# Kernel optimization log

Hardware: AMD Instinct MI355X
Metric: run time of the kernel (lower is better)

Reference implementation:

```python
import jax, jax.numpy as jnp
import numpy as np

B, L, H, NH = 2, 2048, 2048, 16
K = H // NH  # q/k head dim (num_slot) = 128
EPS = 1e-5
SCALE = K ** -0.5  # fla gla default scale = key_dim**-0.5


def setup_inputs() -> dict:
    key = jax.random.key(0)
    k0, k1, k2, k3, k4 = jax.random.split(key, 5)
    std = 0.02
    return {
        "hidden_states": jax.random.normal(k0, (B, L, H), dtype=jnp.float32),
        "Wq": jax.random.normal(k1, (K, H), dtype=jnp.float32) * std,
        "Wk": jax.random.normal(k2, (K, H), dtype=jnp.float32) * std,
        "Wog": jax.random.normal(k3, (H, H), dtype=jnp.float32) * std,
        "Wig": jax.random.normal(k4, (H, H), dtype=jnp.float32) * std,
        "g_weight": jnp.ones((H,), dtype=jnp.float32),
    }


def _gla(q, k, v, g):
    # q,k: [B,L,K]; v: [B,L,V]; g: [B,L,K] (log decay per key dim)
    # recurrence: S_t = exp(g_t)[:, :, None] * S_{t-1} + k_t^T v_t ; o_t = q_t @ S_t
    def step(S, xs):
        q_t, k_t, v_t, g_t = xs  # [B,K],[B,K],[B,V],[B,K]
        S = jnp.exp(g_t)[:, :, None] * S + k_t[:, :, None] * v_t[:, None, :]
        o_t = jnp.einsum('bk,bkv->bv', q_t, S)
        return S, o_t

    S0 = jnp.zeros((q.shape[0], q.shape[2], v.shape[2]), dtype=q.dtype)
    xs = (jnp.swapaxes(q, 0, 1), jnp.swapaxes(k, 0, 1),
          jnp.swapaxes(v, 0, 1), jnp.swapaxes(g, 0, 1))
    _, o = jax.lax.scan(step, S0, xs)  # o: [L,B,V]
    return jnp.swapaxes(o, 0, 1)


def reference(hidden_states, Wq, Wk, Wog, Wig, g_weight):
    x = hidden_states
    q = x @ Wq.T  # [B,L,K]
    k_sig = jax.nn.sigmoid(x @ Wk.T)  # k = sigmoid(k_proj(x))
    q = jax.nn.silu(q) * SCALE  # swish feature map on q; fold in GLA scale
    gf = jax.nn.log_sigmoid(-k_sig)  # per-key log decay gates
    o = _gla(q, k_sig, x, gf)  # [B,L,H] (single head, V = hidden)
    # output gate + fused RMSNorm-SwishGate
    go = o @ Wog.T + x @ Wig.T
    rms = o * jax.lax.rsqrt(jnp.mean(o * o, axis=-1, keepdims=True) + EPS) * g_weight
    return rms * go * jax.nn.sigmoid(go)
```

## Files before the change

kernel.cpp:

```cpp
#include <hip/hip_runtime.h>
#include <math.h>

#define B_ 2
#define L_ 2048
#define H_ 2048
#define KD_ 128
#define SCALE_ 0.08838834764831845f
#define EPS_ 1e-5f
#define K2_ 4096

typedef __bf16 bf16x8 __attribute__((ext_vector_type(8)));
typedef float f32x4 __attribute__((ext_vector_type(4)));

static __device__ __forceinline__ float sigmoidf_(float z) {
    return 1.0f / (1.0f + __expf(-z));
}

static __device__ __forceinline__ unsigned short f2bf(float f) {
    unsigned int u = __float_as_uint(f);
    unsigned int r = (u + 0x7fffu + ((u >> 16) & 1u)) >> 16;
    return (unsigned short)r;
}

static __device__ __forceinline__ float bf2f(unsigned short s) {
    return __uint_as_float(((unsigned int)s) << 16);
}

#define ASYNC_COPY16(gsrc, ldst)                                             \
    __builtin_amdgcn_global_load_lds(                                        \
        (const __attribute__((address_space(1))) unsigned int*)(gsrc),       \
        (__attribute__((address_space(3))) unsigned int*)(ldst), 16, 0, 0)

#define BAR()                                                                \
    do {                                                                     \
        asm volatile("" ::: "memory");                                       \
        __builtin_amdgcn_s_barrier();                                        \
        asm volatile("" ::: "memory");                                       \
    } while (0)

#define JOBA_BLKS 4096
#define JOBB_BLKS 256
#define JOBC_BLKS 4096

__global__ __launch_bounds__(256) void prep_all(
    const float* __restrict__ x, const float* __restrict__ Wq,
    const float* __restrict__ Wk, const float* __restrict__ Wog,
    const float* __restrict__ Wig, unsigned short* __restrict__ Abuf,
    unsigned short* __restrict__ Wqk, unsigned short* __restrict__ Bbuf,
    float* __restrict__ rrms_acc)
{
    const int blk = blockIdx.x;
    const float* src;
    unsigned short* dst;
    if (blk < JOBA_BLKS) {
        size_t i = (size_t)blk * 256 + threadIdx.x;
        size_t m = i >> 8, c8 = (i & 255) * 8;
        src = x + m * H_ + c8;
        dst = Abuf + m * K2_ + H_ + c8;
    } else if (blk < JOBA_BLKS + JOBB_BLKS) {
        size_t i = (size_t)(blk - JOBA_BLKS) * 256 + threadIdx.x;
        if (i < 4096) rrms_acc[i] = 0.f;
        const size_t half = (size_t)KD_ * H_ / 8;
        src = ((i < half) ? Wq : Wk) + ((i < half) ? i : i - half) * 8;
        dst = Wqk + i * 8;
    } else {
        size_t i = (size_t)(blk - JOBA_BLKS - JOBB_BLKS) * 256 + threadIdx.x;
        const size_t half = (size_t)H_ * H_ / 8;
        size_t j = (i < half) ? i : i - half;
        size_t n = j >> 8, c8 = (j & 255) * 8;
        src = ((i < half) ? Wog : Wig) + n * H_ + c8;
        dst = Bbuf + n * K2_ + ((i < half) ? 0 : H_) + c8;
    }
    float4 v0 = *(const float4*)src;
    float4 v1 = *(const float4*)(src + 4);
    ushort4 a, b;
    a.x = f2bf(v0.x); a.y = f2bf(v0.y); a.z = f2bf(v0.z); a.w = f2bf(v0.w);
    b.x = f2bf(v1.x); b.y = f2bf(v1.y); b.z = f2bf(v1.z); b.w = f2bf(v1.w);
    *(ushort4*)dst = a;
    *(ushort4*)(dst + 4) = b;
}

__global__ __launch_bounds__(512, 2) void qk_proj_mfma(
    const unsigned short* __restrict__ Abuf,
    const unsigned short* __restrict__ Wqk,
    float* __restrict__ partial)
{
    __shared__ alignas(16) unsigned short As[3 * 64 * 64];
    __shared__ alignas(16) unsigned short Bs[3 * 256 * 64];
    const int tid  = threadIdx.x;
    const int lane = tid & 63;
    const int w    = tid >> 6;
    const int wrow = w >> 2;
    const int wcol = w & 3;
    const int bid  = blockIdx.x;
    const int m0 = (bid >> 2) * 64;
    const int kz = (bid & 3) * 512;

    const int frow = lane & 15;
    const int fkb  = (lane >> 4) << 3;
    const int rxor = (lane & 7) << 3;

    const int srow = tid >> 3;
    const int scol = (((tid & 7) ^ (srow & 7)) << 3);
    const unsigned short* agsrc =
        Abuf + (size_t)(m0 + srow) * K2_ + H_ + kz + scol;
    const unsigned short* bgsrc = Wqk + (size_t)srow * H_ + kz + scol;
    unsigned short* As_dst = As + tid * 8;
    unsigned short* Bs_dst = Bs + tid * 8;

#define QSTAGE_A_(cb, k0)                                                    \
    ASYNC_COPY16(agsrc + (k0), As_dst + (cb) * 4096)
#define QSTAGE_B_(cb, k0, it_)                                               \
    ASYNC_COPY16(bgsrc + (size_t)((it_) * 64) * H_ + (k0),                   \
                 Bs_dst + (cb) * 16384 + (it_) * 4096)
#define QLDA_(buf, i_, ks_)                                                  \
    (*(const bf16x8*)(As + (buf) * 4096 +                                    \
                      (wrow * 32 + (i_) * 16 + frow) * 64 +                  \
                      (((ks_) * 32 + fkb) ^ rxor)))
#define QLDB_(buf, j_, ks_)                                                  \
    (*(const bf16x8*)(Bs + (buf) * 16384 +                                   \
                      (wcol * 64 + (j_) * 16 + frow) * 64 +                  \
                      (((ks_) * 32 + fkb) ^ rxor)))
#define MFMA_(a_, b_, c_)                                                    \
    (c_) = __builtin_amdgcn_mfma_f32_16x16x32_bf16((a_), (b_), (c_), 0, 0, 0)

    f32x4 acc[2][4] = {};

    QSTAGE_A_(0, 0);
    QSTAGE_B_(0, 0, 0); QSTAGE_B_(0, 0, 1); QSTAGE_B_(0, 0, 2); QSTAGE_B_(0, 0, 3);
    QSTAGE_A_(1, 64);
    QSTAGE_B_(1, 64, 0); QSTAGE_B_(1, 64, 1); QSTAGE_B_(1, 64, 2); QSTAGE_B_(1, 64, 3);
    asm volatile("s_waitcnt vmcnt(5)" ::: "memory");
    BAR();

    int cur = 0;
    for (int t = 0; t < 8; ++t) {
        int stg = cur + 2; if (stg >= 3) stg -= 3;
        const int kpre = (t + 2) * 64;
        const bool pre = (t + 2 < 8);
        bf16x8 af0[2], bf0[4], af1[2], bf1[4];

        #pragma unroll
        for (int i = 0; i < 2; ++i) af0[i] = QLDA_(cur, i, 0);
        #pragma unroll
        for (int j = 0; j < 4; ++j) bf0[j] = QLDB_(cur, j, 0);
        #pragma unroll
        for (int i = 0; i < 2; ++i) af1[i] = QLDA_(cur, i, 1);
        #pragma unroll
        for (int j = 0; j < 4; ++j) bf1[j] = QLDB_(cur, j, 1);

        if (pre) {
            QSTAGE_A_(stg, kpre);
            QSTAGE_B_(stg, kpre, 0);
            QSTAGE_B_(stg, kpre, 1);
            QSTAGE_B_(stg, kpre, 2);
            QSTAGE_B_(stg, kpre, 3);
        }

        __builtin_amdgcn_s_setprio(1);
        #pragma unroll
        for (int i = 0; i < 2; ++i)
            #pragma unroll
            for (int j = 0; j < 4; ++j)
                MFMA_(af0[i], bf0[j], acc[i][j]);
        #pragma unroll
        for (int i = 0; i < 2; ++i)
            #pragma unroll
            for (int j = 0; j < 4; ++j)
                MFMA_(af1[i], bf1[j], acc[i][j]);
        __builtin_amdgcn_s_setprio(0);

        if (pre) { asm volatile("s_waitcnt vmcnt(5)" ::: "memory"); }
        else     { asm volatile("s_waitcnt vmcnt(0)" ::: "memory"); }
        BAR();

        cur = cur + 1; if (cur == 3) cur = 0;
    }

#undef QSTAGE_A_
#undef QSTAGE_B_
#undef QLDA_
#undef QLDB_
#undef MFMA_

    float* pz = partial + (size_t)(bid & 3) * 4096 * 256;
    #pragma unroll
    for (int i = 0; i < 2; ++i) {
        #pragma unroll
        for (int reg = 0; reg < 4; ++reg) {
            int m = m0 + wrow * 32 + i * 16 + (lane >> 4) * 4 + reg;
            #pragma unroll
            for (int j = 0; j < 4; ++j) {
                int n = wcol * 64 + j * 16 + (lane & 15);
                pz[(size_t)m * 256 + n] = acc[i][j][reg];
            }
        }
    }
}

__global__ __launch_bounds__(256) void scan_scale_kernel(
    const float* __restrict__ partial,
    unsigned short* __restrict__ qt_b, unsigned short* __restrict__ kA_b,
    unsigned short* __restrict__ kB_b)
{
    const int c = blockIdx.x, b = blockIdx.y;
    const int kd = blockIdx.z * 32 + (threadIdx.x & 31);
    const int rg = threadIdx.x >> 5;
    const size_t stride = (size_t)4096 * 256;
    const int row0 = b * L_ + c * 64 + rg * 8;

    float qv[8], kv[8], gp[8];
    float run = 0.f;
    #pragma unroll
    for (int j = 0; j < 8; ++j) {
        size_t off = (size_t)(row0 + j) * 256;
        float sq = partial[off + kd] + partial[stride + off + kd]
                 + partial[2 * stride + off + kd] + partial[3 * stride + off + kd];
        float sk = partial[off + 128 + kd] + partial[stride + off + 128 + kd]
                 + partial[2 * stride + off + 128 + kd]
                 + partial[3 * stride + off + 128 + kd];
        float ksv = sigmoidf_(sk);
        qv[j] = sq * sigmoidf_(sq) * SCALE_;
        kv[j] = ksv;
        run += -log1pf(__expf(ksv));
        gp[j] = run;
    }
    __shared__ float s_seg[8][32];
    s_seg[rg][threadIdx.x & 31] = run;
    __syncthreads();
    float base = 0.f, total = 0.f;
    #pragma unroll
    for (int r = 0; r < 8; ++r) {
        float v = s_seg[r][threadIdx.x & 31];
        base += (r < rg) ? v : 0.f;
        total += v;
    }
    #pragma unroll
    for (int j = 0; j < 8; ++j) {
        float s = base + gp[j];
        size_t idx = (size_t)(row0 + j) * KD_ + kd;
        qt_b[idx] = f2bf(qv[j] * __expf(s));
        kA_b[idx] = f2bf(kv[j] * __expf(-s));
        kB_b[idx] = f2bf(kv[j] * __expf(total - s));
    }
}

#define SV_ 130
#define SP_ 136

__global__ __launch_bounds__(256) void pv_fused(
    const unsigned short* __restrict__ qt_b,
    const unsigned short* __restrict__ kA_b,
    const unsigned short* __restrict__ kB_b,
    unsigned short* Abuf,
    float* __restrict__ rrms_acc)
{
    const int c  = blockIdx.x;
    const int b  = blockIdx.y;
    const int vg = blockIdx.z;
    const int tid = threadIdx.x;
    const int w = tid >> 6, l = tid & 63;
    const int lr = l & 15, lq = l >> 4;
    const int q0 = c * 64, kpos0 = q0 - 64;
    const size_t rowbase = (size_t)b * L_;

    __shared__ alignas(16) unsigned short Pl[64 * SP_];
    __shared__ alignas(16) unsigned short Vt[128 * SV_];

    {
        bf16x8 aq[4];
        const unsigned short* qrow = qt_b + (rowbase + q0 + 16 * w + lr) * KD_;
        #pragma unroll
        for (int kt = 0; kt < 4; ++kt)
            aq[kt] = *(const bf16x8*)(qrow + kt * 32 + lq * 8);
        #pragma unroll
        for (int jt = 0; jt < 8; ++jt) {
            f32x4 p = {};
            const int si = jt * 16 + lr;
            const bool prev = (jt < 4);
            const bool dead = (c == 0 && prev);
            if (!dead) {
                int kp = prev ? (q0 - 64 + si) : (q0 + si - 64);
                const unsigned short* kb =
                    (prev ? kB_b : kA_b) + (rowbase + kp) * KD_;
                #pragma unroll
                for (int kt = 0; kt < 4; ++kt) {
                    bf16x8 bk = *(const bf16x8*)(kb + kt * 32 + lq * 8);
                    p = __builtin_amdgcn_mfma_f32_16x16x32_bf16(aq[kt], bk, p,
                                                                0, 0, 0);
                }
            }
            #pragma unroll
            for (int reg = 0; reg < 4; ++reg) {
                int ti = 16 * w + lq * 4 + reg;
                bool keep = !dead && (si <= ti + 64);
                Pl[ti * SP_ + si] = keep ? f2bf(p[reg]) : (unsigned short)0;
            }
        }
    }
    __syncthreads();

    bf16x8 ap[4];
    #pragma unroll
    for (int kt = 0; kt < 4; ++kt)
        ap[kt] = *(const bf16x8*)(Pl + (16 * w + lr) * SP_ + kt * 32 + lq * 8);

    float rsum[4] = {0.f, 0.f, 0.f, 0.f};

    #pragma unroll
    for (int h = 0; h < 2; ++h) {
        const int vt = vg * 2 + h;
        const int v0c = vt * 128;
        if (h) __syncthreads();

        {
            const int a = tid & 15;
            const int kr0 = tid >> 4;
            for (int kr = kr0; kr < 128; kr += 16) {
                int kp = kpos0 + kr;
                ushort4 u0 = {0, 0, 0, 0}, u1 = {0, 0, 0, 0};
                if (kp >= 0) {
                    const unsigned short* src =
                        Abuf + (rowbase + kp) * K2_ + H_ + v0c + a * 8;
                    u0 = *(const ushort4*)src;
                    u1 = *(const ushort4*)(src + 4);
                }
                unsigned short vals[8] = {u0.x, u0.y, u0.z, u0.w,
                                          u1.x, u1.y, u1.z, u1.w};
                #pragma unroll
                for (int j = 0; j < 8; ++j)
                    Vt[(a * 8 + j) * SV_ + kr] = vals[j];
            }
        }
        __syncthreads();

        #pragma unroll
        for (int jt = 0; jt < 8; ++jt) {
            f32x4 oa = {};
            const int n = jt * 16 + lr;
            #pragma unroll
            for (int kt = 0; kt < 4; ++kt) {
                const unsigned int* vp =
                    (const unsigned int*)(Vt + n * SV_ + kt * 32 + lq * 8);
                union { unsigned int u[4]; bf16x8 v; } bb;
                bb.u[0] = vp[0]; bb.u[1] = vp[1];
                bb.u[2] = vp[2]; bb.u[3] = vp[3];
                oa = __builtin_amdgcn_mfma_f32_16x16x32_bf16(ap[kt], bb.v, oa,
                                                             0, 0, 0);
            }
            #pragma unroll
            for (int reg = 0; reg < 4; ++reg) {
                int qrow = 16 * w + lq * 4 + reg;
                size_t orow = rowbase + q0 + qrow;
                float val = oa[reg];
                Abuf[orow * K2_ + v0c + n] = f2bf(val);
                rsum[reg] += val * val;
            }
        }
    }

    #pragma unroll
    for (int mk = 1; mk < 16; mk <<= 1) {
        #pragma unroll
        for (int reg = 0; reg < 4; ++reg)
            rsum[reg] += __shfl_xor(rsum[reg], mk, 64);
    }
    if (lr == 0) {
        #pragma unroll
        for (int reg = 0; reg < 4; ++reg)
            atomicAdd(&rrms_acc[rowbase + q0 + 16 * w + lq * 4 + reg], rsum[reg]);
    }
}

__global__ __launch_bounds__(512, 2) void out_gemm_mfma(
    const unsigned short* __restrict__ Abuf,
    const unsigned short* __restrict__ Bbuf,
    const float* __restrict__ gw, const float* __restrict__ rrms_acc,
    float* __restrict__ out)
{
    __shared__ alignas(16) unsigned short As[3 * 128 * 64];
    __shared__ alignas(16) unsigned short Bs[3 * 256 * 64];
    const int tid  = threadIdx.x;
    const int lane = tid & 63;
    const int w    = tid >> 6;
    const int wrow = w >> 2;
    const int wcol = w & 3;
    const int bid  = blockIdx.x;
    const int m0 = (bid >> 3) * 128;
    const int n0 = (bid & 7) * 256;

    const int frow = lane & 15;
    const int fkb  = (lane >> 4) << 3;
    const int rxor = (lane & 7) << 3;

    const int srow = tid >> 3;
    const int scol = (((tid & 7) ^ (srow & 7)) << 3);
    const unsigned short* agsrc = Abuf + (size_t)(m0 + srow) * K2_ + scol;
    const unsigned short* bgsrc = Bbuf + (size_t)(n0 + srow) * K2_ + scol;
    unsigned short* As_dst = As + tid * 8;
    unsigned short* Bs_dst = Bs + tid * 8;

#define STAGE_A2_(cb, k0)                                                    \
    {                                                                        \
        ASYNC_COPY16(agsrc + (k0), As_dst + (cb) * 8192);                    \
        ASYNC_COPY16(agsrc + (size_t)64 * K2_ + (k0),                        \
                     As_dst + (cb) * 8192 + 4096);                           \
    }
#define STAGE_B1_(cb, k0, it_)                                               \
    ASYNC_COPY16(bgsrc + (size_t)((it_) * 64) * K2_ + (k0),                  \
                 Bs_dst + (cb) * 16384 + (it_) * 4096)
#define LDA_(buf, i_, ks_)                                                   \
    (*(const bf16x8*)(As + (buf) * 8192 +                                    \
                      (wrow * 64 + (i_) * 16 + frow) * 64 +                  \
                      (((ks_) * 32 + fkb) ^ rxor)))
#define LDB_(buf, j_, ks_)                                                   \
    (*(const bf16x8*)(Bs + (buf) * 16384 +                                   \
                      (wcol * 64 + (j_) * 16 + frow) * 64 +                  \
                      (((ks_) * 32 + fkb) ^ rxor)))
#define MFMA_(a_, b_, c_)                                                    \
    (c_) = __builtin_amdgcn_mfma_f32_16x16x32_bf16((a_), (b_), (c_), 0, 0, 0)

    f32x4 acc[4][4] = {};

    STAGE_A2_(0, 0);
    STAGE_B1_(0, 0, 0); STAGE_B1_(0, 0, 1); STAGE_B1_(0, 0, 2); STAGE_B1_(0, 0, 3);
    STAGE_A2_(1, 64);
    STAGE_B1_(1, 64, 0); STAGE_B1_(1, 64, 1); STAGE_B1_(1, 64, 2); STAGE_B1_(1, 64, 3);
    asm volatile("s_waitcnt vmcnt(6)" ::: "memory");
    BAR();

    int cur = 0;
    for (int t = 0; t < 64; ++t) {
        int stg = cur + 2; if (stg >= 3) stg -= 3;
        const int kpre = (t + 2) * 64;
        const bool pre = (t + 2 < 64);
        bf16x8 af0[4], bf0[4], af1[4], bf1[4];

        #pragma unroll
        for (int i = 0; i < 4; ++i) af0[i] = LDA_(cur, i, 0);
        #pragma unroll
        for (int j = 0; j < 4; ++j) bf0[j] = LDB_(cur, j, 0);
        #pragma unroll
        for (int i = 0; i < 4; ++i) af1[i] = LDA_(cur, i, 1);
        #pragma unroll
        for (int j = 0; j < 4; ++j) bf1[j] = LDB_(cur, j, 1);

        if (pre) {
            STAGE_A2_(stg, kpre);
            STAGE_B1_(stg, kpre, 0);
            STAGE_B1_(stg, kpre, 1);
            STAGE_B1_(stg, kpre, 2);
            STAGE_B1_(stg, kpre, 3);
        }

        __builtin_amdgcn_s_setprio(1);
        #pragma unroll
        for (int i = 0; i < 4; ++i)
            #pragma unroll
            for (int j = 0; j < 4; ++j)
                MFMA_(af0[i], bf0[j], acc[i][j]);
        #pragma unroll
        for (int i = 0; i < 4; ++i)
            #pragma unroll
            for (int j = 0; j < 4; ++j)
                MFMA_(af1[i], bf1[j], acc[i][j]);
        __builtin_amdgcn_s_setprio(0);

        if (pre) { asm volatile("s_waitcnt vmcnt(6)" ::: "memory"); }
        else     { asm volatile("s_waitcnt vmcnt(0)" ::: "memory"); }
        BAR();

        cur = cur + 1; if (cur == 3) cur = 0;
    }

#undef STAGE_A2_
#undef STAGE_B1_
#undef LDA_
#undef LDB_
#undef MFMA_

    #pragma unroll
    for (int i = 0; i < 4; ++i) {
        #pragma unroll
        for (int reg = 0; reg < 4; ++reg) {
            int m = m0 + wrow * 64 + i * 16 + (lane >> 4) * 4 + reg;
            float rv = rsqrtf(rrms_acc[m] * (1.0f / H_) + EPS_);
            #pragma unroll
            for (int j = 0; j < 4; ++j) {
                int n = n0 + wcol * 64 + j * 16 + (lane & 15);
                float go = acc[i][j][reg];
                float ov = bf2f(Abuf[(size_t)m * K2_ + n]);
                out[(size_t)m * H_ + n] = ov * rv * gw[n] * go * sigmoidf_(go);
            }
        }
    }
}

extern "C" void kernel_launch(void* const* d_in, const int* in_sizes, int n_in,
                              void* d_out, int out_size, void* d_ws, size_t ws_size,
                              hipStream_t stream) {
    (void)in_sizes; (void)n_in; (void)out_size; (void)ws_size;
    const float* x   = (const float*)d_in[0];
    const float* Wq  = (const float*)d_in[1];
    const float* Wk  = (const float*)d_in[2];
    const float* Wog = (const float*)d_in[3];
    const float* Wig = (const float*)d_in[4];
    const float* gw  = (const float*)d_in[5];
    float* out = (float*)d_out;

    const size_t MK = (size_t)B_ * L_ * KD_;
    unsigned short* Abuf = (unsigned short*)d_ws;
    unsigned short* Bbuf = Abuf + (size_t)4096 * K2_;
    unsigned short* qt_b = Bbuf + (size_t)2048 * K2_;
    unsigned short* kA_b = qt_b + MK;
    unsigned short* kB_b = kA_b + MK;
    unsigned short* Wqk  = kB_b + MK;
    unsigned short* Pbuf = Wqk + (size_t)256 * H_;
    float* partial  = (float*)(Pbuf + (size_t)64 * 64 * 128);
    float* rrms_acc = partial + (size_t)4 * 4096 * 256;

    prep_all<<<JOBA_BLKS + JOBB_BLKS + JOBC_BLKS, 256, 0, stream>>>(
        x, Wq, Wk, Wog, Wig, Abuf, Wqk, Bbuf, rrms_acc);
    qk_proj_mfma<<<256, 512, 0, stream>>>(Abuf, Wqk, partial);
    scan_scale_kernel<<<dim3(32, B_, 4), 256, 0, stream>>>(partial, qt_b, kA_b, kB_b);
    pv_fused<<<dim3(32, B_, 8), 256, 0, stream>>>(qt_b, kA_b, kB_b, Abuf, rrms_acc);
    out_gemm_mfma<<<256, 512, 0, stream>>>(Abuf, Bbuf, gw, rrms_acc, out);
}
```

Baseline: 232.1 us.

## Fuse five kernels into one cooperative persistent kernel with grid syncs

Merges the prep, qk-projection, scan/scale, pv and output-GEMM kernels into one cooperative-launched kernel of 256 blocks of 512 threads. Stages are separated by grid.sync and share one static LDS buffer. The goal is to remove the per-launch overhead and the idle tail between the five launches. In exchange, every stage is locked to the same grid shape. The scan stage leaves half the threads idle, the prep stage loops with fewer threads, and the larger shared buffer may limit occupancy.

```diff
diff --git a/kernel.cpp b/kernel.cpp
--- a/kernel.cpp
+++ b/kernel.cpp
@@ -1,5 +1,8 @@
 #include <hip/hip_runtime.h>
+#include <hip/hip_cooperative_groups.h>
 #include <math.h>
+
+namespace cg = cooperative_groups;
 
 #define B_ 2
 #define L_ 2048
@@ -38,75 +41,84 @@
         asm volatile("" ::: "memory");                                       \
     } while (0)
 
-#define JOBA_BLKS 4096
-#define JOBB_BLKS 256
-#define JOBC_BLKS 4096
-
-__global__ __launch_bounds__(256) void prep_all(
+#define SV_ 130
+#define SP_ 136
+
+__global__ __launch_bounds__(512, 2) void gla_mega(
     const float* __restrict__ x, const float* __restrict__ Wq,
     const float* __restrict__ Wk, const float* __restrict__ Wog,
-    const float* __restrict__ Wig, unsigned short* __restrict__ Abuf,
-    unsigned short* __restrict__ Wqk, unsigned short* __restrict__ Bbuf,
-    float* __restrict__ rrms_acc)
+    const float* __restrict__ Wig, const float* __restrict__ gw,
+    unsigned short* Abuf, unsigned short* __restrict__ Wqk,
+    unsigned short* __restrict__ Bbuf, float* __restrict__ partial,
+    unsigned short* __restrict__ qt_b, unsigned short* __restrict__ kA_b,
+    unsigned short* __restrict__ kB_b, float* rrms_acc,
+    float* __restrict__ out)
 {
-    const int blk = blockIdx.x;
-    const float* src;
-    unsigned short* dst;
-    if (blk < JOBA_BLKS) {
-        size_t i = (size_t)blk * 256 + threadIdx.x;
-        size_t m = i >> 8, c8 = (i & 255) * 8;
-        src = x + m * H_ + c8;
-        dst = Abuf + m * K2_ + H_ + c8;
-    } else if (blk < JOBA_BLKS + JOBB_BLKS) {
-        size_t i = (size_t)(blk - JOBA_BLKS) * 256 + threadIdx.x;
-        if (i < 4096) rrms_acc[i] = 0.f;
-        const size_t half = (size_t)KD_ * H_ / 8;
-        src = ((i < half) ? Wq : Wk) + ((i < half) ? i : i - half) * 8;
-        dst = Wqk + i * 8;
-    } else {
-        size_t i = (size_t)(blk - JOBA_BLKS - JOBB_BLKS) * 256 + threadIdx.x;
-        const size_t half = (size_t)H_ * H_ / 8;
-        size_t j = (i < half) ? i : i - half;
-        size_t n = j >> 8, c8 = (j & 255) * 8;
-        src = ((i < half) ? Wog : Wig) + n * H_ + c8;
-        dst = Bbuf + n * K2_ + ((i < half) ? 0 : H_) + c8;
+    cg::grid_group grid = cg::this_grid();
+    __shared__ alignas(16) unsigned short SMEM[73728];
+    const int tid = threadIdx.x;
+    const int bid = blockIdx.x;
+    const int lane = tid & 63;
+
+    {
+        const size_t NA = 1048576;
+        const size_t NB = 65536;
+        const size_t NC = 1048576;
+        const size_t gtid = (size_t)bid * 512 + tid;
+        for (size_t idx = gtid; idx < NA + NB + NC; idx += 131072) {
+            const float* src;
+            unsigned short* dst;
+            if (idx < NA) {
+                size_t m = idx >> 8, c8 = (idx & 255) * 8;
+                src = x + m * H_ + c8;
+                dst = Abuf + m * K2_ + H_ + c8;
+            } else if (idx < NA + NB) {
+                size_t i = idx - NA;
+                if (i < 4096) rrms_acc[i] = 0.f;
+                const size_t half = (size_t)KD_ * H_ / 8;
+                src = ((i < half) ? Wq : Wk) + ((i < half) ? i : i - half) * 8;
+                dst = Wqk + i * 8;
+            } else {
+                size_t i = idx - NA - NB;
+                const size_t half = (size_t)H_ * H_ / 8;
+                size_t j = (i < half) ? i : i - half;
+                size_t n = j >> 8, c8 = (j & 255) * 8;
+                src = ((i < half) ? Wog : Wig) + n * H_ + c8;
+                dst = Bbuf + n * K2_ + ((i < half) ? 0 : H_) + c8;
+            }
+            float4 v0 = *(const float4*)src;
+            float4 v1 = *(const float4*)(src + 4);
+            ushort4 a, b;
+            a.x = f2bf(v0.x); a.y = f2bf(v0.y);
+            a.z = f2bf(v0.z); a.w = f2bf(v0.w);
+            b.x = f2bf(v1.x); b.y = f2bf(v1.y);
+            b.z = f2bf(v1.z); b.w = f2bf(v1.w);
+            *(ushort4*)dst = a;
+            *(ushort4*)(dst + 4) = b;
+        }
     }
-    float4 v0 = *(const float4*)src;
-    float4 v1 = *(const float4*)(src + 4);
-    ushort4 a, b;
-    a.x = f2bf(v0.x); a.y = f2bf(v0.y); a.z = f2bf(v0.z); a.w = f2bf(v0.w);
-    b.x = f2bf(v1.x); b.y = f2bf(v1.y); b.z = f2bf(v1.z); b.w = f2bf(v1.w);
-    *(ushort4*)dst = a;
-    *(ushort4*)(dst + 4) = b;
-}
-
-__global__ __launch_bounds__(512, 2) void qk_proj_mfma(
-    const unsigned short* __restrict__ Abuf,
-    const unsigned short* __restrict__ Wqk,
-    float* __restrict__ partial)
-{
-    __shared__ alignas(16) unsigned short As[3 * 64 * 64];
-    __shared__ alignas(16) unsigned short Bs[3 * 256 * 64];
-    const int tid  = threadIdx.x;
-    const int lane = tid & 63;
-    const int w    = tid >> 6;
-    const int wrow = w >> 2;
-    const int wcol = w & 3;
-    const int bid  = blockIdx.x;
-    const int m0 = (bid >> 2) * 64;
-    const int kz = (bid & 3) * 512;
-
-    const int frow = lane & 15;
-    const int fkb  = (lane >> 4) << 3;
-    const int rxor = (lane & 7) << 3;
-
-    const int srow = tid >> 3;
-    const int scol = (((tid & 7) ^ (srow & 7)) << 3);
-    const unsigned short* agsrc =
-        Abuf + (size_t)(m0 + srow) * K2_ + H_ + kz + scol;
-    const unsigned short* bgsrc = Wqk + (size_t)srow * H_ + kz + scol;
-    unsigned short* As_dst = As + tid * 8;
-    unsigned short* Bs_dst = Bs + tid * 8;
+    grid.sync();
+
+    {
+        unsigned short* const As = &SMEM[0];
+        unsigned short* const Bs = &SMEM[12288];
+        const int w    = tid >> 6;
+        const int wrow = w >> 2;
+        const int wcol = w & 3;
+        const int m0 = (bid >> 2) * 64;
+        const int kz = (bid & 3) * 512;
+
+        const int frow = lane & 15;
+        const int fkb  = (lane >> 4) << 3;
+        const int rxor = (lane & 7) << 3;
+
+        const int srow = tid >> 3;
+        const int scol = (((tid & 7) ^ (srow & 7)) << 3);
+        const unsigned short* agsrc =
+            Abuf + (size_t)(m0 + srow) * K2_ + H_ + kz + scol;
+        const unsigned short* bgsrc = Wqk + (size_t)srow * H_ + kz + scol;
+        unsigned short* As_dst = As + tid * 8;
+        unsigned short* Bs_dst = Bs + tid * 8;
 
 #define QSTAGE_A_(cb, k0)                                                    \
     ASYNC_COPY16(agsrc + (k0), As_dst + (cb) * 4096)
@@ -124,58 +136,60 @@
 #define MFMA_(a_, b_, c_)                                                    \
     (c_) = __builtin_amdgcn_mfma_f32_16x16x32_bf16((a_), (b_), (c_), 0, 0, 0)
 
-    f32x4 acc[2][4] = {};
-
-    QSTAGE_A_(0, 0);
-    QSTAGE_B_(0, 0, 0); QSTAGE_B_(0, 0, 1); QSTAGE_B_(0, 0, 2); QSTAGE_B_(0, 0, 3);
-    QSTAGE_A_(1, 64);
-    QSTAGE_B_(1, 64, 0); QSTAGE_B_(1, 64, 1); QSTAGE_B_(1, 64, 2); QSTAGE_B_(1, 64, 3);
-    asm volatile("s_waitcnt vmcnt(5)" ::: "memory");
-    BAR();
-
-    int cur = 0;
-    for (int t = 0; t < 8; ++t) {
-        int stg = cur + 2; if (stg >= 3) stg -= 3;
-        const int kpre = (t + 2) * 64;
-        const bool pre = (t + 2 < 8);
-        bf16x8 af0[2], bf0[4], af1[2], bf1[4];
-
-        #pragma unroll
-        for (int i = 0; i < 2; ++i) af0[i] = QLDA_(cur, i, 0);
-        #pragma unroll
-        for (int j = 0; j < 4; ++j) bf0[j] = QLDB_(cur, j, 0);
-        #pragma unroll
-        for (int i = 0; i < 2; ++i) af1[i] = QLDA_(cur, i, 1);
-        #pragma unroll
-        for (int j = 0; j < 4; ++j) bf1[j] = QLDB_(cur, j, 1);
-
-        if (pre) {
-            QSTAGE_A_(stg, kpre);
-            QSTAGE_B_(stg, kpre, 0);
-            QSTAGE_B_(stg, kpre, 1);
-            QSTAGE_B_(stg, kpre, 2);
-            QSTAGE_B_(stg, kpre, 3);
-        }
-
-        __builtin_amdgcn_s_setprio(1);
-        #pragma unroll
-        for (int i = 0; i < 2; ++i)
-            #pragma unroll
-            for (int j = 0; j < 4; ++j)
-                MFMA_(af0[i], bf0[j], acc[i][j]);
-        #pragma unroll
-        for (int i = 0; i < 2; ++i)
-            #pragma unroll
-            for (int j = 0; j < 4; ++j)
-                MFMA_(af1[i], bf1[j], acc[i][j]);
-        __builtin_amdgcn_s_setprio(0);
-
-        if (pre) { asm volatile("s_waitcnt vmcnt(5)" ::: "memory"); }
-        else     { asm volatile("s_waitcnt vmcnt(0)" ::: "memory"); }
+        f32x4 acc[2][4] = {};
+
+        QSTAGE_A_(0, 0);
+        QSTAGE_B_(0, 0, 0); QSTAGE_B_(0, 0, 1);
+        QSTAGE_B_(0, 0, 2); QSTAGE_B_(0, 0, 3);
+        QSTAGE_A_(1, 64);
+        QSTAGE_B_(1, 64, 0); QSTAGE_B_(1, 64, 1);
+        QSTAGE_B_(1, 64, 2); QSTAGE_B_(1, 64, 3);
+        asm volatile("s_waitcnt vmcnt(5)" ::: "memory");
         BAR();
 
-        cur = cur + 1; if (cur == 3) cur = 0;
-    }
+        int cur = 0;
+        for (int t = 0; t < 8; ++t) {
+            int stg = cur + 2; if (stg >= 3) stg -= 3;
+            const int kpre = (t + 2) * 64;
+            const bool pre = (t + 2 < 8);
+            bf16x8 af0[2], bf0[4], af1[2], bf1[4];
+
+            #pragma unroll
+            for (int i = 0; i < 2; ++i) af0[i] = QLDA_(cur, i, 0);
+            #pragma unroll
+            for (int j = 0; j < 4; ++j) bf0[j] = QLDB_(cur, j, 0);
+            #pragma unroll
+            for (int i = 0; i < 2; ++i) af1[i] = QLDA_(cur, i, 1);
+            #pragma unroll
+            for (int j = 0; j < 4; ++j) bf1[j] = QLDB_(cur, j, 1);
+
+            if (pre) {
+                QSTAGE_A_(stg, kpre);
+                QSTAGE_B_(stg, kpre, 0);
+                QSTAGE_B_(stg, kpre, 1);
+                QSTAGE_B_(stg, kpre, 2);
+                QSTAGE_B_(stg, kpre, 3);
+            }
+
+            __builtin_amdgcn_s_setprio(1);
+            #pragma unroll
+            for (int i = 0; i < 2; ++i)
+                #pragma unroll
+                for (int j = 0; j < 4; ++j)
+                    MFMA_(af0[i], bf0[j], acc[i][j]);
+            #pragma unroll
+            for (int i = 0; i < 2; ++i)
+                #pragma unroll
+                for (int j = 0; j < 4; ++j)
+                    MFMA_(af1[i], bf1[j], acc[i][j]);
+            __builtin_amdgcn_s_setprio(0);
+
+            if (pre) { asm volatile("s_waitcnt vmcnt(5)" ::: "memory"); }
+            else     { asm volatile("s_waitcnt vmcnt(0)" ::: "memory"); }
+            BAR();
+
+            cur = cur + 1; if (cur == 3) cur = 0;
+        }
 
 #undef QSTAGE_A_
 #undef QSTAGE_B_
@@ -183,222 +197,213 @@
 #undef QLDB_
 #undef MFMA_
 
-    float* pz = partial + (size_t)(bid & 3) * 4096 * 256;
-    #pragma unroll
-    for (int i = 0; i < 2; ++i) {
+        float* pz = partial + (size_t)(bid & 3) * 4096 * 256;
         #pragma unroll
-        for (int reg = 0; reg < 4; ++reg) {
-            int m = m0 + wrow * 32 + i * 16 + (lane >> 4) * 4 + reg;
-            #pragma unroll
-            for (int j = 0; j < 4; ++j) {
-                int n = wcol * 64 + j * 16 + (lane & 15);
-                pz[(size_t)m * 256 + n] = acc[i][j][reg];
+        for (int i = 0; i < 2; ++i) {
+            #pragma unroll
+            for (int reg = 0; reg < 4; ++reg) {
+                int m = m0 + wrow * 32 + i * 16 + (lane >> 4) * 4 + reg;
+                #pragma unroll
+                for (int j = 0; j < 4; ++j) {
+                    int n = wcol * 64 + j * 16 + (lane & 15);
+                    pz[(size_t)m * 256 + n] = acc[i][j][reg];
+                }
             }
         }
     }
-}
-
-__global__ __launch_bounds__(256) void scan_scale_kernel(
-    const float* __restrict__ partial,
-    unsigned short* __restrict__ qt_b, unsigned short* __restrict__ kA_b,
-    unsigned short* __restrict__ kB_b)
-{
-    const int c = blockIdx.x, b = blockIdx.y;
-    const int kd = blockIdx.z * 32 + (threadIdx.x & 31);
-    const int rg = threadIdx.x >> 5;
-    const size_t stride = (size_t)4096 * 256;
-    const int row0 = b * L_ + c * 64 + rg * 8;
-
-    float qv[8], kv[8], gp[8];
-    float run = 0.f;
-    #pragma unroll
-    for (int j = 0; j < 8; ++j) {
-        size_t off = (size_t)(row0 + j) * 256;
-        float sq = partial[off + kd] + partial[stride + off + kd]
-                 + partial[2 * stride + off + kd] + partial[3 * stride + off + kd];
-        float sk = partial[off + 128 + kd] + partial[stride + off + 128 + kd]
-                 + partial[2 * stride + off + 128 + kd]
-                 + partial[3 * stride + off + 128 + kd];
-        float ksv = sigmoidf_(sk);
-        qv[j] = sq * sigmoidf_(sq) * SCALE_;
-        kv[j] = ksv;
-        run += -log1pf(__expf(ksv));
-        gp[j] = run;
+    grid.sync();
+
+    {
+        float* const s_seg = (float*)&SMEM[0];
+        const bool act = (tid < 256);
+        const int c = bid & 31, b = (bid >> 5) & 1, z = bid >> 6;
+        const int kd = z * 32 + (tid & 31);
+        const int rg = (tid >> 5) & 7;
+        const size_t stride = (size_t)4096 * 256;
+        const int row0 = b * L_ + c * 64 + rg * 8;
+
+        float qv[8], kv[8], gp[8];
+        float run = 0.f, base = 0.f, total = 0.f;
+        if (act) {
+            #pragma unroll
+            for (int j = 0; j < 8; ++j) {
+                size_t off = (size_t)(row0 + j) * 256;
+                float sq = partial[off + kd] + partial[stride + off + kd]
+                         + partial[2 * stride + off + kd]
+                         + partial[3 * stride + off + kd];
+                float sk = partial[off + 128 + kd]
+                         + partial[stride + off + 128 + kd]
+                         + partial[2 * stride + off + 128 + kd]
+                         + partial[3 * stride + off + 128 + kd];
+                float ksv = sigmoidf_(sk);
+                qv[j] = sq * sigmoidf_(sq) * SCALE_;
+                kv[j] = ksv;
+                run += -log1pf(__expf(ksv));
+                gp[j] = run;
+            }
+            s_seg[rg * 32 + (tid & 31)] = run;
+        }
+        __syncthreads();
+        if (act) {
+            #pragma unroll
+            for (int r = 0; r < 8; ++r) {
+                float v = s_seg[r * 32 + (tid & 31)];
+                base += (r < rg) ? v : 0.f;
+                total += v;
+            }
+            #pragma unroll
+            for (int j = 0; j < 8; ++j) {
+                float s = base + gp[j];
+                size_t idx = (size_t)(row0 + j) * KD_ + kd;
+                qt_b[idx] = f2bf(qv[j] * __expf(s));
+                kA_b[idx] = f2bf(kv[j] * __expf(-s));
+                kB_b[idx] = f2bf(kv[j] * __expf(total - s));
+            }
+        }
     }
-    __shared__ float s_seg[8][32];
-    s_seg[rg][threadIdx.x & 31] = run;
-    __syncthreads();
-    float base = 0.f, total = 0.f;
-    #pragma unroll
-    for (int r = 0; r < 8; ++r) {
-        float v = s_seg[r][threadIdx.x & 31];
-        base += (r < rg) ? v : 0.f;
-        total += v;
-    }
-    #pragma unroll
-    for (int j = 0; j < 8; ++j) {
-        float s = base + gp[j];
-        size_t idx = (size_t)(row0 + j) * KD_ + kd;
-        qt_b[idx] = f2bf(qv[j] * __expf(s));
-        kA_b[idx] = f2bf(kv[j] * __expf(-s));
-        kB_b[idx] = f2bf(kv[j] * __expf(total - s));
-    }
-}
-
-#define SV_ 130
-#define SP_ 136
-
-__global__ __launch_bounds__(256) void pv_fused(
-    const unsigned short* __restrict__ qt_b,
-    const unsigned short* __restrict__ kA_b,
-    const unsigned short* __restrict__ kB_b,
-    unsigned short* Abuf,
-    float* __restrict__ rrms_acc)
-{
-    const int c  = blockIdx.x;
-    const int b  = blockIdx.y;
-    const int vg = blockIdx.z;
-    const int tid = threadIdx.x;
-    const int w = tid >> 6, l = tid & 63;
-    const int lr = l & 15, lq = l >> 4;
-    const int q0 = c * 64, kpos0 = q0 - 64;
-    const size_t rowbase = (size_t)b * L_;
-
-    __shared__ alignas(16) unsigned short Pl[64 * SP_];
-    __shared__ alignas(16) unsigned short Vt[128 * SV_];
+    grid.sync();
 
     {
-        bf16x8 aq[4];
-        const unsigned short* qrow = qt_b + (rowbase + q0 + 16 * w + lr) * KD_;
+        const int half = tid >> 8;
+        const int t = tid & 255;
+        const int u = (bid << 1) | half;
+        const int c = u & 31, b = (u >> 5) & 1, vg = u >> 6;
+        const int w = t >> 6, l = t & 63;
+        const int lr = l & 15, lq = l >> 4;
+        const int q0 = c * 64, kpos0 = q0 - 64;
+        const size_t rowbase = (size_t)b * L_;
+
+        unsigned short* const Pl = &SMEM[(size_t)half * 25344];
+        unsigned short* const Vt = &SMEM[(size_t)half * 25344 + 8704];
+
+        {
+            bf16x8 aq[4];
+            const unsigned short* qrow =
+                qt_b + (rowbase + q0 + 16 * w + lr) * KD_;
+            #pragma unroll
+            for (int kt = 0; kt < 4; ++kt)
+                aq[kt] = *(const bf16x8*)(qrow + kt * 32 + lq * 8);
+            #pragma unroll
+            for (int jt = 0; jt < 8; ++jt) {
+                f32x4 p = {};
+                const int si = jt * 16 + lr;
+                const bool prev = (jt < 4);
+                const bool dead = (c == 0 && prev);
+                if (!dead) {
+                    int kp = prev ? (q0 - 64 + si) : (q0 + si - 64);
+                    const unsigned short* kb =
+                        (prev ? kB_b : kA_b) + (rowbase + kp) * KD_;
+                    #pragma unroll
+                    for (int kt = 0; kt < 4; ++kt) {
+                        bf16x8 bk = *(const bf16x8*)(kb + kt * 32 + lq * 8);
+                        p = __builtin_amdgcn_mfma_f32_16x16x32_bf16(
+                            aq[kt], bk, p, 0, 0, 0);
+                    }
+                }
+                #pragma unroll
+                for (int reg = 0; reg < 4; ++reg) {
+                    int ti = 16 * w + lq * 4 + reg;
+                    bool keep = !dead && (si <= ti + 64);
+                    Pl[ti * SP_ + si] = keep ? f2bf(p[reg]) : (unsigned short)0;
+                }
+            }
+        }
+        __syncthreads();
+
+        bf16x8 ap[4];
         #pragma unroll
         for (int kt = 0; kt < 4; ++kt)
-            aq[kt] = *(const bf16x8*)(qrow + kt * 32 + lq * 8);
+            ap[kt] = *(const bf16x8*)(Pl + (16 * w + lr) * SP_ +
+                                      kt * 32 + lq * 8);
+
+        float rsum[4] = {0.f, 0.f, 0.f, 0.f};
+
         #pragma unroll
-        for (int jt = 0; jt < 8; ++jt) {
-            f32x4 p = {};
-            const int si = jt * 16 + lr;
-            const bool prev = (jt < 4);
-            const bool dead = (c == 0 && prev);
-            if (!dead) {
-                int kp = prev ? (q0 - 64 + si) : (q0 + si - 64);
-                const unsigned short* kb =
-                    (prev ? kB_b : kA_b) + (rowbase + kp) * KD_;
+        for (int h = 0; h < 2; ++h) {
+            const int vt = vg * 2 + h;
+            const int v0c = vt * 128;
+            if (h) __syncthreads();
+
+            {
+                const int a = t & 15;
+                const int kr0 = t >> 4;
+                for (int kr = kr0; kr < 128; kr += 16) {
+                    int kp = kpos0 + kr;
+                    ushort4 u0 = {0, 0, 0, 0}, u1 = {0, 0, 0, 0};
+                    if (kp >= 0) {
+                        const unsigned short* src =
+                            Abuf + (rowbase + kp) * K2_ + H_ + v0c + a * 8;
+                        u0 = *(const ushort4*)src;
+                        u1 = *(const ushort4*)(src + 4);
+                    }
+                    unsigned short vals[8] = {u0.x, u0.y, u0.z, u0.w,
+                                              u1.x, u1.y, u1.z, u1.w};
+                    #pragma unroll
+                    for (int j = 0; j < 8; ++j)
+                        Vt[(a * 8 + j) * SV_ + kr] = vals[j];
+                }
+            }
+            __syncthreads();
+
+            #pragma unroll
+            for (int jt = 0; jt < 8; ++jt) {
+                f32x4 oa = {};
+                const int n = jt * 16 + lr;
                 #pragma unroll
                 for (int kt = 0; kt < 4; ++kt) {
-                    bf16x8 bk = *(const bf16x8*)(kb + kt * 32 + lq * 8);
-                    p = __builtin_amdgcn_mfma_f32_16x16x32_bf16(aq[kt], bk, p,
-                                                                0, 0, 0);
-                }
-            }
-            #pragma unroll
-            for (int reg = 0; reg < 4; ++reg) {
-                int ti = 16 * w + lq * 4 + reg;
-                bool keep = !dead && (si <= ti + 64);
-                Pl[ti * SP_ + si] = keep ? f2bf(p[reg]) : (unsigned short)0;
-            }
+                    const unsigned int* vp =
+                        (const unsigned int*)(Vt + n * SV_ + kt * 32 + lq * 8);
+                    union { unsigned int uu[4]; bf16x8 v; } bb;
+                    bb.uu[0] = vp[0]; bb.uu[1] = vp[1];
+                    bb.uu[2] = vp[2]; bb.uu[3] = vp[3];
+                    oa = __builtin_amdgcn_mfma_f32_16x16x32_bf16(
+                        ap[kt], bb.v, oa, 0, 0, 0);
+                }
+                #pragma unroll
+                for (int reg = 0; reg < 4; ++reg) {
+                    int qrow = 16 * w + lq * 4 + reg;
+                    size_t orow = rowbase + q0 + qrow;
+                    float val = oa[reg];
+                    Abuf[orow * K2_ + v0c + n] = f2bf(val);
+                    rsum[reg] += val * val;
+                }
+            }
+        }
+
+        #pragma unroll
+        for (int mk = 1; mk < 16; mk <<= 1) {
+            #pragma unroll
+            for (int reg = 0; reg < 4; ++reg)
+                rsum[reg] += __shfl_xor(rsum[reg], mk, 64);
+        }
+        if (lr == 0) {
+            #pragma unroll
+            for (int reg = 0; reg < 4; ++reg)
+                atomicAdd(&rrms_acc[rowbase + q0 + 16 * w + lq * 4 + reg],
+                          rsum[reg]);
         }
     }
-    __syncthreads();
-
-    bf16x8 ap[4];
-    #pragma unroll
-    for (int kt = 0; kt < 4; ++kt)
-        ap[kt] = *(const bf16x8*)(Pl + (16 * w + lr) * SP_ + kt * 32 + lq * 8);
-
-    float rsum[4] = {0.f, 0.f, 0.f, 0.f};
-
-    #pragma unroll
-    for (int h = 0; h < 2; ++h) {
-        const int vt = vg * 2 + h;
-        const int v0c = vt * 128;
-        if (h) __syncthreads();
-
-        {
-            const int a = tid & 15;
-            const int kr0 = tid >> 4;
-            for (int kr = kr0; kr < 128; kr += 16) {
-                int kp = kpos0 + kr;
-                ushort4 u0 = {0, 0, 0, 0}, u1 = {0, 0, 0, 0};
-                if (kp >= 0) {
-                    const unsigned short* src =
-                        Abuf + (rowbase + kp) * K2_ + H_ + v0c + a * 8;
-                    u0 = *(const ushort4*)src;
-                    u1 = *(const ushort4*)(src + 4);
-                }
-                unsigned short vals[8] = {u0.x, u0.y, u0.z, u0.w,
-                                          u1.x, u1.y, u1.z, u1.w};
-                #pragma unroll
-                for (int j = 0; j < 8; ++j)
-                    Vt[(a * 8 + j) * SV_ + kr] = vals[j];
-            }
-        }
-        __syncthreads();
-
-        #pragma unroll
-        for (int jt = 0; jt < 8; ++jt) {
-            f32x4 oa = {};
-            const int n = jt * 16 + lr;
-            #pragma unroll
-            for (int kt = 0; kt < 4; ++kt) {
-                const unsigned int* vp =
-                    (const unsigned int*)(Vt + n * SV_ + kt * 32 + lq * 8);
-                union { unsigned int u[4]; bf16x8 v; } bb;
-                bb.u[0] = vp[0]; bb.u[1] = vp[1];
-                bb.u[2] = vp[2]; bb.u[3] = vp[3];
-                oa = __builtin_amdgcn_mfma_f32_16x16x32_bf16(ap[kt], bb.v, oa,
-                                                             0, 0, 0);
-            }
-            #pragma unroll
-            for (int reg = 0; reg < 4; ++reg) {
-                int qrow = 16 * w + lq * 4 + reg;
-                size_t orow = rowbase + q0 + qrow;
-                float val = oa[reg];
-                Abuf[orow * K2_ + v0c + n] = f2bf(val);
-                rsum[reg] += val * val;
-            }
-        }
-    }
-
-    #pragma unroll
-    for (int mk = 1; mk < 16; mk <<= 1) {
-        #pragma unroll
-        for (int reg = 0; reg < 4; ++reg)
-            rsum[reg] += __shfl_xor(rsum[reg], mk, 64);
-    }
-    if (lr == 0) {
-        #pragma unroll
-        for (int reg = 0; reg < 4; ++reg)
-            atomicAdd(&rrms_acc[rowbase + q0 + 16 * w + lq * 4 + reg], rsum[reg]);
-    }
-}
-
-__global__ __launch_bounds__(512, 2) void out_gemm_mfma(
-    const unsigned short* __restrict__ Abuf,
-    const unsigned short* __restrict__ Bbuf,
-    const float* __restrict__ gw, const float* __restrict__ rrms_acc,
-    float* __restrict__ out)
-{
-    __shared__ alignas(16) unsigned short As[3 * 128 * 64];
-    __shared__ alignas(16) unsigned short Bs[3 * 256 * 64];
-    const int tid  = threadIdx.x;
-    const int lane = tid & 63;
-    const int w    = tid >> 6;
-    const int wrow = w >> 2;
-    const int wcol = w & 3;
-    const int bid  = blockIdx.x;
-    const int m0 = (bid >> 3) * 128;
-    const int n0 = (bid & 7) * 256;
-
-    const int frow = lane & 15;
-    const int fkb  = (lane >> 4) << 3;
-    const int rxor = (lane & 7) << 3;
-
-    const int srow = tid >> 3;
-    const int scol = (((tid & 7) ^ (srow & 7)) << 3);
-    const unsigned short* agsrc = Abuf + (size_t)(m0 + srow) * K2_ + scol;
-    const unsigned short* bgsrc = Bbuf + (size_t)(n0 + srow) * K2_ + scol;
-    unsigned short* As_dst = As + tid * 8;
-    unsigned short* Bs_dst = Bs + tid * 8;
+    grid.sync();
+
+    {
+        unsigned short* const As = &SMEM[0];
+        unsigned short* const Bs = &SMEM[24576];
+        const int w    = tid >> 6;
+        const int wrow = w >> 2;
+        const int wcol = w & 3;
+        const int m0 = (bid >> 3) * 128;
+        const int n0 = (bid & 7) * 256;
+
+        const int frow = lane & 15;
+        const int fkb  = (lane >> 4) << 3;
+        const int rxor = (lane & 7) << 3;
+
+        const int srow = tid >> 3;
+        const int scol = (((tid & 7) ^ (srow & 7)) << 3);
+        const unsigned short* agsrc = Abuf + (size_t)(m0 + srow) * K2_ + scol;
+        const unsigned short* bgsrc = Bbuf + (size_t)(n0 + srow) * K2_ + scol;
+        unsigned short* As_dst = As + tid * 8;
+        unsigned short* Bs_dst = Bs + tid * 8;
 
 #define STAGE_A2_(cb, k0)                                                    \
     {                                                                        \
@@ -420,58 +425,60 @@
 #define MFMA_(a_, b_, c_)                                                    \
     (c_) = __builtin_amdgcn_mfma_f32_16x16x32_bf16((a_), (b_), (c_), 0, 0, 0)
 
-    f32x4 acc[4][4] = {};
-
-    STAGE_A2_(0, 0);
-    STAGE_B1_(0, 0, 0); STAGE_B1_(0, 0, 1); STAGE_B1_(0, 0, 2); STAGE_B1_(0, 0, 3);
-    STAGE_A2_(1, 64);
-    STAGE_B1_(1, 64, 0); STAGE_B1_(1, 64, 1); STAGE_B1_(1, 64, 2); STAGE_B1_(1, 64, 3);
-    asm volatile("s_waitcnt vmcnt(6)" ::: "memory");
-    BAR();
-
-    int cur = 0;
-    for (int t = 0; t < 64; ++t) {
-        int stg = cur + 2; if (stg >= 3) stg -= 3;
-        const int kpre = (t + 2) * 64;
-        const bool pre = (t + 2 < 64);
-        bf16x8 af0[4], bf0[4], af1[4], bf1[4];
-
-        #pragma unroll
-        for (int i = 0; i < 4; ++i) af0[i] = LDA_(cur, i, 0);
-        #pragma unroll
-        for (int j = 0; j < 4; ++j) bf0[j] = LDB_(cur, j, 0);
-        #pragma unroll
-        for (int i = 0; i < 4; ++i) af1[i] = LDA_(cur, i, 1);
-        #pragma unroll
-        for (int j = 0; j < 4; ++j) bf1[j] = LDB_(cur, j, 1);
-
-        if (pre) {
-            STAGE_A2_(stg, kpre);
-            STAGE_B1_(stg, kpre, 0);
-            STAGE_B1_(stg, kpre, 1);
-            STAGE_B1_(stg, kpre, 2);
-            STAGE_B1_(stg, kpre, 3);
-        }
-
-        __builtin_amdgcn_s_setprio(1);
-        #pragma unroll
-        for (int i = 0; i < 4; ++i)
-            #pragma unroll
-            for (int j = 0; j < 4; ++j)
-                MFMA_(af0[i], bf0[j], acc[i][j]);
-        #pragma unroll
-        for (int i = 0; i < 4; ++i)
-            #pragma unroll
-            for (int j = 0; j < 4; ++j)
-                MFMA_(af1[i], bf1[j], acc[i][j]);
-        __builtin_amdgcn_s_setprio(0);
-
-        if (pre) { asm volatile("s_waitcnt vmcnt(6)" ::: "memory"); }
-        else     { asm volatile("s_waitcnt vmcnt(0)" ::: "memory"); }
+        f32x4 acc[4][4] = {};
+
+        STAGE_A2_(0, 0);
+        STAGE_B1_(0, 0, 0); STAGE_B1_(0, 0, 1);
+        STAGE_B1_(0, 0, 2); STAGE_B1_(0, 0, 3);
+        STAGE_A2_(1, 64);
+        STAGE_B1_(1, 64, 0); STAGE_B1_(1, 64, 1);
+        STAGE_B1_(1, 64, 2); STAGE_B1_(1, 64, 3);
+        asm volatile("s_waitcnt vmcnt(6)" ::: "memory");
         BAR();
 
-        cur = cur + 1; if (cur == 3) cur = 0;
-    }
+        int cur = 0;
+        for (int t = 0; t < 64; ++t) {
+            int stg = cur + 2; if (stg >= 3) stg -= 3;
+            const int kpre = (t + 2) * 64;
+            const bool pre = (t + 2 < 64);
+            bf16x8 af0[4], bf0[4], af1[4], bf1[4];
+
+            #pragma unroll
+            for (int i = 0; i < 4; ++i) af0[i] = LDA_(cur, i, 0);
+            #pragma unroll
+            for (int j = 0; j < 4; ++j) bf0[j] = LDB_(cur, j, 0);
+            #pragma unroll
+            for (int i = 0; i < 4; ++i) af1[i] = LDA_(cur, i, 1);
+            #pragma unroll
+            for (int j = 0; j < 4; ++j) bf1[j] = LDB_(cur, j, 1);
+
+            if (pre) {
+                STAGE_A2_(stg, kpre);
+                STAGE_B1_(stg, kpre, 0);
+                STAGE_B1_(stg, kpre, 1);
+                STAGE_B1_(stg, kpre, 2);
+                STAGE_B1_(stg, kpre, 3);
+            }
+
+            __builtin_amdgcn_s_setprio(1);
+            #pragma unroll
+            for (int i = 0; i < 4; ++i)
+                #pragma unroll
+                for (int j = 0; j < 4; ++j)
+                    MFMA_(af0[i], bf0[j], acc[i][j]);
+            #pragma unroll
+            for (int i = 0; i < 4; ++i)
+                #pragma unroll
+                for (int j = 0; j < 4; ++j)
+                    MFMA_(af1[i], bf1[j], acc[i][j]);
+            __builtin_amdgcn_s_setprio(0);
+
+            if (pre) { asm volatile("s_waitcnt vmcnt(6)" ::: "memory"); }
+            else     { asm volatile("s_waitcnt vmcnt(0)" ::: "memory"); }
+            BAR();
+
+            cur = cur + 1; if (cur == 3) cur = 0;
+        }
 
 #undef STAGE_A2_
 #undef STAGE_B1_
@@ -479,18 +486,20 @@
 #undef LDB_
 #undef MFMA_
 
-    #pragma unroll
-    for (int i = 0; i < 4; ++i) {
         #pragma unroll
-        for (int reg = 0; reg < 4; ++reg) {
-            int m = m0 + wrow * 64 + i * 16 + (lane >> 4) * 4 + reg;
-            float rv = rsqrtf(rrms_acc[m] * (1.0f / H_) + EPS_);
-            #pragma unroll
-            for (int j = 0; j < 4; ++j) {
-                int n = n0 + wcol * 64 + j * 16 + (lane & 15);
-                float go = acc[i][j][reg];
-                float ov = bf2f(Abuf[(size_t)m * K2_ + n]);
-                out[(size_t)m * H_ + n] = ov * rv * gw[n] * go * sigmoidf_(go);
+        for (int i = 0; i < 4; ++i) {
+            #pragma unroll
+            for (int reg = 0; reg < 4; ++reg) {
+                int m = m0 + wrow * 64 + i * 16 + (lane >> 4) * 4 + reg;
+                float rv = rsqrtf(rrms_acc[m] * (1.0f / H_) + EPS_);
+                #pragma unroll
+                for (int j = 0; j < 4; ++j) {
+                    int n = n0 + wcol * 64 + j * 16 + (lane & 15);
+                    float go = acc[i][j][reg];
+                    float ov = bf2f(Abuf[(size_t)m * K2_ + n]);
+                    out[(size_t)m * H_ + n] =
+                        ov * rv * gw[n] * go * sigmoidf_(go);
+                }
             }
         }
     }
@@ -519,10 +528,11 @@
     float* partial  = (float*)(Pbuf + (size_t)64 * 64 * 128);
     float* rrms_acc = partial + (size_t)4 * 4096 * 256;
 
-    prep_all<<<JOBA_BLKS + JOBB_BLKS + JOBC_BLKS, 256, 0, stream>>>(
-        x, Wq, Wk, Wog, Wig, Abuf, Wqk, Bbuf, rrms_acc);
-    qk_proj_mfma<<<256, 512, 0, stream>>>(Abuf, Wqk, partial);
-    scan_scale_kernel<<<dim3(32, B_, 4), 256, 0, stream>>>(partial, qt_b, kA_b, kB_b);
-    pv_fused<<<dim3(32, B_, 8), 256, 0, stream>>>(qt_b, kA_b, kB_b, Abuf, rrms_acc);
-    out_gemm_mfma<<<256, 512, 0, stream>>>(Abuf, Bbuf, gw, rrms_acc, out);
+    void* kargs[] = {
+        (void*)&x, (void*)&Wq, (void*)&Wk, (void*)&Wog, (void*)&Wig,
+        (void*)&gw, (void*)&Abuf, (void*)&Wqk, (void*)&Bbuf,
+        (void*)&partial, (void*)&qt_b, (void*)&kA_b, (void*)&kB_b,
+        (void*)&rrms_acc, (void*)&out};
+    hipLaunchCooperativeKernel((const void*)gla_mega, dim3(256), dim3(512),
+                               kargs, 0, stream);
 }
```

Result: slower. 371.2 us (+59.9%).
